# Performance work log

Measured on AMD Instinct MI355X. Metric: run time of the kernel, lower is better.

Reference implementation:

```python
import jax, jax.numpy as jnp
import numpy as np

B, T, E = 4, 1024, 1024
H, MULT = 16, 2
HD = E // H
SCALE = HD ** -0.5


def setup_inputs() -> dict:
    key = jax.random.key(0)
    ks = jax.random.split(key, 9)
    s = 0.02
    return {
        "hidden_states": jax.random.normal(ks[0], (B, T, E), jnp.float32),
        "attention_mask": jnp.zeros((B, 1, T, T), jnp.float32),
        "Wq": jax.random.normal(ks[1], (E, E), jnp.float32) * s,
        "bq": jnp.zeros((E,), jnp.float32),
        "Wk": jax.random.normal(ks[2], (MULT * E, E), jnp.float32) * s,
        "bk": jnp.zeros((MULT * E,), jnp.float32),
        "Wv": jax.random.normal(ks[3], (MULT * E, E), jnp.float32) * s,
        "bv": jnp.zeros((MULT * E,), jnp.float32),
        "Wo": jax.random.normal(ks[4], (E, E), jnp.float32) * s,
        "bo": jnp.zeros((E,), jnp.float32),
    }


def reference(hidden_states, attention_mask, Wq, bq, Wk, bk, Wv, bv, Wo, bo):
    x = hidden_states  # [B, T, E]
    # q projection, scaled
    q = (jnp.einsum("bte,fe->btf", x, Wq) + bq) * SCALE  # [B,T,E]
    q = q.reshape(B, T, H, HD).transpose(0, 2, 1, 3)      # [B,H,T,HD]
    # k/v project to multiplier-expanded dim, then _shape with seq_len=-1:
    # [B,T,MULT*E] -> view(B, T*MULT, H, HD) (torch view semantics) -> [B,H,T*MULT,HD]
    k = jnp.einsum("bte,fe->btf", x, Wk) + bk             # [B,T,MULT*E]
    k = k.reshape(B, T * MULT, H, HD).transpose(0, 2, 1, 3)
    v = jnp.einsum("bte,fe->btf", x, Wv) + bv
    v = v.reshape(B, T * MULT, H, HD).transpose(0, 2, 1, 3)

    S = T * MULT  # src_len; src_len0 = T
    attn = jnp.einsum("bhtd,bhsd->bhts", q, k)            # [B,H,T,S]
    # custom mask broadcast: view src as [MULT, src_len0] and add mask[:, :, :, None, :]
    attn = attn.reshape(B, H, T, MULT, T) + attention_mask[:, :, :, None, :]
    attn = attn.reshape(B, H, T, S)
    attn = jax.nn.softmax(attn, axis=-1)
    out = jnp.einsum("bhts,bhsd->bhtd", attn, v)          # [B,H,T,HD]
    out = out.transpose(0, 2, 1, 3).reshape(B, T, E)
    out = jnp.einsum("bte,fe->btf", out, Wo) + bo
    return out
```

## Files before the change

kernel.cpp:

```cpp
#include <hip/hip_runtime.h>
#include <math.h>

#define BB    4
#define TT    1024
#define EE    1024
#define HH    16
#define HDIM  64
#define SS    2048
#define MROWS 4096
#define SCALEQ 0.125f

typedef short  s8v  __attribute__((ext_vector_type(8)));
typedef float  f4v  __attribute__((ext_vector_type(4)));

__device__ __forceinline__ unsigned short f2bf(float f) {
    union { float f; unsigned u; } c; c.f = f;
    unsigned u = c.u + 0x7FFFu + ((c.u >> 16) & 1u);
    return (unsigned short)(u >> 16);
}
__device__ __forceinline__ float bf2f(unsigned short h) {
    union { unsigned u; float f; } c; c.u = ((unsigned)h) << 16;
    return c.f;
}

__device__ __forceinline__ void async16(const void* g, void* l) {
    __builtin_amdgcn_global_load_lds(
        (const __attribute__((address_space(1))) unsigned int*)g,
        (__attribute__((address_space(3))) unsigned int*)l,
        16, 0, 0);
}

__global__ __launch_bounds__(256) void cvt6_kernel(
    const float* __restrict__ x,  const float* __restrict__ wq,
    const float* __restrict__ wk, const float* __restrict__ wv,
    const float* __restrict__ wo, const float* __restrict__ mk,
    unsigned short* __restrict__ xb,  unsigned short* __restrict__ wqb,
    unsigned short* __restrict__ wkb, unsigned short* __restrict__ wvb,
    unsigned short* __restrict__ wob, unsigned short* __restrict__ mbb)
{
    const int total = 3670016;
    int i = blockIdx.x * 256 + threadIdx.x;
    const int stride = gridDim.x * 256;
    for (; i < total; i += stride) {
        const float* s; unsigned short* d; int off;
        if (i < 1048576)      { s = x;  d = xb;  off = i; }
        else if (i < 1310720) { s = wq; d = wqb; off = i - 1048576; }
        else if (i < 1835008) { s = wk; d = wkb; off = i - 1310720; }
        else if (i < 2359296) { s = wv; d = wvb; off = i - 1835008; }
        else if (i < 2621440) { s = wo; d = wob; off = i - 2359296; }
        else                  { s = mk; d = mbb; off = i - 2621440; }
        float4 v = ((const float4*)s)[off];
        ushort4 o;
        o.x = f2bf(v.x); o.y = f2bf(v.y); o.z = f2bf(v.z); o.w = f2bf(v.w);
        ((ushort4*)d)[off] = o;
    }
}

#define GEMM_KLOOP(Aptr, Wptr, Ksz)                                            \
    for (int k0 = 0; k0 < (Ksz); k0 += 32) {                                   \
        _Pragma("unroll")                                                      \
        for (int it = 0; it < 2; ++it) {                                       \
            int f = (it * 4 + w) * 64 + lane;                                  \
            int r = f >> 2, g = (f & 3) * 8;                                   \
            async16((Aptr) + (size_t)(m0 + r) * (Ksz) + k0 + g,                \
                    As + (it * 4 + w) * 512);                                  \
            async16((Wptr) + (size_t)(n0 + r) * (Ksz) + k0 + g,                \
                    Bs + (it * 4 + w) * 512);                                  \
        }                                                                      \
        __syncthreads();                                                       \
        s8v af[4], bf[4];                                                      \
        _Pragma("unroll")                                                      \
        for (int i = 0; i < 4; ++i)                                            \
            af[i] = *(const s8v*)(As + (wm + i * 16 + col16) * 32 + quad * 8); \
        _Pragma("unroll")                                                      \
        for (int j = 0; j < 4; ++j)                                            \
            bf[j] = *(const s8v*)(Bs + (wn + j * 16 + col16) * 32 + quad * 8); \
        _Pragma("unroll")                                                      \
        for (int i = 0; i < 4; ++i)                                            \
            _Pragma("unroll")                                                  \
            for (int j = 0; j < 4; ++j)                                        \
                acc[i][j] = __builtin_amdgcn_mfma_f32_16x16x32_bf16(           \
                    af[i], bf[j], acc[i][j], 0, 0, 0);                         \
        __syncthreads();                                                       \
    }

__global__ __launch_bounds__(256, 3) void gemm_qk_kernel(
    const unsigned short* __restrict__ X,  const unsigned short* __restrict__ Wq,
    const unsigned short* __restrict__ Wk, const float* __restrict__ bq,
    const float* __restrict__ bk, unsigned short* __restrict__ qp,
    unsigned short* __restrict__ kp)
{
    __shared__ __align__(16) unsigned short As[128 * 32];
    __shared__ __align__(16) unsigned short Bs[128 * 32];

    const int tid = threadIdx.x;
    const int lane = tid & 63, w = tid >> 6;
    const int wm = (w & 1) * 64, wn = (w >> 1) * 64;
    const int col16 = lane & 15, quad = lane >> 4;
    const int m0 = blockIdx.x * 128;
    const bool isQ = blockIdx.y < 8;
    const int n0 = blockIdx.y * 128;
    const unsigned short* Wrow = isQ ? Wq + (size_t)n0 * EE
                                     : Wk + (size_t)(n0 - EE) * EE;

    f4v acc[4][4];
#pragma unroll
    for (int i = 0; i < 4; ++i)
#pragma unroll
        for (int j = 0; j < 4; ++j) acc[i][j] = (f4v)0.0f;

    for (int k0 = 0; k0 < EE; k0 += 32) {
#pragma unroll
        for (int it = 0; it < 2; ++it) {
            int f = (it * 4 + w) * 64 + lane;
            int r = f >> 2, g = (f & 3) * 8;
            async16(X + (size_t)(m0 + r) * EE + k0 + g, As + (it * 4 + w) * 512);
            async16(Wrow + (size_t)r * EE + k0 + g, Bs + (it * 4 + w) * 512);
        }
        __syncthreads();
        s8v af[4], bf[4];
#pragma unroll
        for (int i = 0; i < 4; ++i)
            af[i] = *(const s8v*)(As + (wm + i * 16 + col16) * 32 + quad * 8);
#pragma unroll
        for (int j = 0; j < 4; ++j)
            bf[j] = *(const s8v*)(Bs + (wn + j * 16 + col16) * 32 + quad * 8);
#pragma unroll
        for (int i = 0; i < 4; ++i)
#pragma unroll
            for (int j = 0; j < 4; ++j)
                acc[i][j] = __builtin_amdgcn_mfma_f32_16x16x32_bf16(
                    af[i], bf[j], acc[i][j], 0, 0, 0);
        __syncthreads();
    }

#pragma unroll
    for (int j = 0; j < 4; ++j) {
        const int n = n0 + wn + j * 16 + col16;
        const float bn = isQ ? bq[n] : bk[n - EE];
#pragma unroll
        for (int i = 0; i < 4; ++i) {
            const int mb = m0 + wm + i * 16 + quad * 4;
#pragma unroll
            for (int r = 0; r < 4; ++r) {
                const int m = mb + r;
                float c = acc[i][j][r] + bn;
                if (isQ) {
                    qp[(size_t)m * EE + n] = f2bf(c * SCALEQ);
                } else {
                    const int nk = n - EE;
                    const int mm = nk >> 10, h = (nk >> 6) & 15, d = nk & 63;
                    const int b_ = m >> 10, t = m & 1023;
                    const int s = 2 * t + mm;
                    kp[((size_t)(b_ * HH + h) * SS + s) * HDIM + d] = f2bf(c);
                }
            }
        }
    }
}

template <int LAYOUT, int OUTF32, int Ksz, int Nsz>
__global__ __launch_bounds__(256, 3) void gemm_mfma_kernel(
    const unsigned short* __restrict__ A, const unsigned short* __restrict__ W,
    const float* __restrict__ bias, void* __restrict__ Cout, float alpha)
{
    __shared__ __align__(16) unsigned short As[128 * 32];
    __shared__ __align__(16) unsigned short Bs[128 * 32];

    const int tid = threadIdx.x;
    const int lane = tid & 63, w = tid >> 6;
    const int wm = (w & 1) * 64, wn = (w >> 1) * 64;
    const int col16 = lane & 15, quad = lane >> 4;
    const int m0 = blockIdx.x * 128;
    const int n0 = blockIdx.y * 128;

    f4v acc[4][4];
#pragma unroll
    for (int i = 0; i < 4; ++i)
#pragma unroll
        for (int j = 0; j < 4; ++j) acc[i][j] = (f4v)0.0f;

    GEMM_KLOOP(A, W, Ksz)

#pragma unroll
    for (int j = 0; j < 4; ++j) {
        const int n = n0 + wn + j * 16 + col16;
        const float bn = (LAYOUT == 2) ? 0.0f : bias[n];
#pragma unroll
        for (int i = 0; i < 4; ++i) {
            const int mb = m0 + wm + i * 16 + quad * 4;
#pragma unroll
            for (int r = 0; r < 4; ++r) {
                const int m = mb + r;
                float c = (acc[i][j][r] + ((LAYOUT == 2) ? bias[m] : bn)) * alpha;
                if (LAYOUT == 0) {
                    if (OUTF32) ((float*)Cout)[(size_t)m * Nsz + n] = c;
                    else ((unsigned short*)Cout)[(size_t)m * Nsz + n] = f2bf(c);
                } else {
                    const int mm = m >> 10, h = (m >> 6) & 15, d = m & 63;
                    const int b_ = n >> 10, t = n & 1023;
                    const int s = 2 * t + mm;
                    ((unsigned short*)Cout)[((size_t)(b_ * HH + h) * HDIM + d) * SS + s] = f2bf(c);
                }
            }
        }
    }
}

__global__ __launch_bounds__(256, 3) void attn_mfma2_kernel(
    const unsigned short* __restrict__ Q, const unsigned short* __restrict__ Kh,
    const unsigned short* __restrict__ Vt, const unsigned short* __restrict__ Mb,
    unsigned short* __restrict__ O)
{
    constexpr int PT = 68;
    __shared__ __align__(16) unsigned short Qs[64 * PT];
    __shared__ __align__(16) unsigned short K0[64 * PT];
    __shared__ __align__(16) unsigned short K1[64 * PT];
    __shared__ __align__(16) unsigned short V0[64 * PT];
    __shared__ __align__(16) unsigned short V1[64 * PT];
    __shared__ __align__(16) unsigned short Ms[64 * PT];

    const int tid = threadIdx.x;
    const int lane = tid & 63, w = tid >> 6;
    const int col16 = lane & 15, quad = lane >> 4;

    const int gid = blockIdx.x;
    const int v = gid & 7, j = gid >> 3;
    const int bh = v * 8 + (j >> 4);
    const int t0 = (j & 15) * 64;
    const int b_ = bh >> 4, h = bh & 15;

#pragma unroll
    for (int it = 0; it < 2; ++it) {
        int idx = tid + it * 256;
        int r = idx >> 3, c = (idx & 7) * 8;
        *(uint4*)(Qs + r * PT + c) =
            *(const uint4*)(Q + (size_t)(b_ * TT + t0 + r) * EE + h * HDIM + c);
    }

    f4v oacc[4];
#pragma unroll
    for (int jd = 0; jd < 4; ++jd) oacc[jd] = (f4v)0.0f;
    float mrun = -INFINITY, lrun = 0.0f;

    const unsigned short* Kb  = Kh + (size_t)bh * SS * HDIM;
    const unsigned short* Vb  = Vt + (size_t)bh * HDIM * SS;
    const unsigned short* Mbb = Mb + (size_t)b_ * TT * TT;
    const int myrow = (w * 16 + col16) * PT;

    for (int it16 = 0; it16 < 16; ++it16) {
        const int t2b = it16 * 64;
        __syncthreads();
#pragma unroll
        for (int st = 0; st < 2; ++st) {
            int idx = tid + st * 256;
            int r = idx >> 3, c = (idx & 7) * 8;
            *(uint4*)(K0 + r * PT + c) = *(const uint4*)(Kb + (size_t)(t2b + r) * HDIM + c);
            *(uint4*)(K1 + r * PT + c) = *(const uint4*)(Kb + (size_t)(1024 + t2b + r) * HDIM + c);
            *(uint4*)(V0 + r * PT + c) = *(const uint4*)(Vb + (size_t)r * SS + t2b + c);
            *(uint4*)(V1 + r * PT + c) = *(const uint4*)(Vb + (size_t)r * SS + 1024 + t2b + c);
            *(uint4*)(Ms + r * PT + c) = *(const uint4*)(Mbb + (size_t)(t0 + r) * TT + t2b + c);
        }
        __syncthreads();

        f4v s0acc[4], s1acc[4];
#pragma unroll
        for (int js = 0; js < 4; ++js) { s0acc[js] = (f4v)0.0f; s1acc[js] = (f4v)0.0f; }
#pragma unroll
        for (int ks = 0; ks < 2; ++ks) {
            s8v bq_ = *(const s8v*)(Qs + myrow + ks * 32 + quad * 8);
#pragma unroll
            for (int js = 0; js < 4; ++js) {
                s8v ak0 = *(const s8v*)(K0 + (js * 16 + col16) * PT + ks * 32 + quad * 8);
                s8v ak1 = *(const s8v*)(K1 + (js * 16 + col16) * PT + ks * 32 + quad * 8);
                s0acc[js] = __builtin_amdgcn_mfma_f32_16x16x32_bf16(ak0, bq_, s0acc[js], 0, 0, 0);
                s1acc[js] = __builtin_amdgcn_mfma_f32_16x16x32_bf16(ak1, bq_, s1acc[js], 0, 0, 0);
            }
        }

#pragma unroll
        for (int js = 0; js < 4; ++js) {
            uint2 mm = *(const uint2*)(Ms + myrow + js * 16 + quad * 4);
            float m0f = bf2f((unsigned short)(mm.x & 0xffff));
            float m1f = bf2f((unsigned short)(mm.x >> 16));
            float m2f = bf2f((unsigned short)(mm.y & 0xffff));
            float m3f = bf2f((unsigned short)(mm.y >> 16));
            s0acc[js][0] += m0f; s1acc[js][0] += m0f;
            s0acc[js][1] += m1f; s1acc[js][1] += m1f;
            s0acc[js][2] += m2f; s1acc[js][2] += m2f;
            s0acc[js][3] += m3f; s1acc[js][3] += m3f;
        }

        float tmax = -INFINITY;
#pragma unroll
        for (int js = 0; js < 4; ++js)
#pragma unroll
            for (int r = 0; r < 4; ++r)
                tmax = fmaxf(tmax, fmaxf(s0acc[js][r], s1acc[js][r]));
        tmax = fmaxf(tmax, __shfl_xor(tmax, 16));
        tmax = fmaxf(tmax, __shfl_xor(tmax, 32));
        const float mnew = fmaxf(mrun, tmax);
        const float scl = __expf(mrun - mnew);
        float rs = 0.0f;
#pragma unroll
        for (int js = 0; js < 4; ++js)
#pragma unroll
            for (int r = 0; r < 4; ++r) {
                float p0 = __expf(s0acc[js][r] - mnew);
                float p1 = __expf(s1acc[js][r] - mnew);
                s0acc[js][r] = p0; s1acc[js][r] = p1;
                rs += p0 + p1;
            }
        rs += __shfl_xor(rs, 16);
        rs += __shfl_xor(rs, 32);
        lrun = lrun * scl + rs;
        mrun = mnew;

        float sclr[4];
#pragma unroll
        for (int r = 0; r < 4; ++r) sclr[r] = __shfl(scl, quad * 4 + r);
#pragma unroll
        for (int jd = 0; jd < 4; ++jd)
#pragma unroll
            for (int r = 0; r < 4; ++r) oacc[jd][r] *= sclr[r];

        __syncthreads();

#pragma unroll
        for (int js = 0; js < 4; ++js) {
            unsigned p01 = (unsigned)f2bf(s0acc[js][0]) | ((unsigned)f2bf(s0acc[js][1]) << 16);
            unsigned p23 = (unsigned)f2bf(s0acc[js][2]) | ((unsigned)f2bf(s0acc[js][3]) << 16);
            *(uint2*)(K0 + myrow + js * 16 + quad * 4) = make_uint2(p01, p23);
            p01 = (unsigned)f2bf(s1acc[js][0]) | ((unsigned)f2bf(s1acc[js][1]) << 16);
            p23 = (unsigned)f2bf(s1acc[js][2]) | ((unsigned)f2bf(s1acc[js][3]) << 16);
            *(uint2*)(K1 + myrow + js * 16 + quad * 4) = make_uint2(p01, p23);
        }
        __syncthreads();

#pragma unroll
        for (int ks = 0; ks < 2; ++ks) {
            s8v p0 = *(const s8v*)(K0 + myrow + ks * 32 + quad * 8);
            s8v p1 = *(const s8v*)(K1 + myrow + ks * 32 + quad * 8);
#pragma unroll
            for (int jd = 0; jd < 4; ++jd) {
                s8v v0_ = *(const s8v*)(V0 + (jd * 16 + col16) * PT + ks * 32 + quad * 8);
                s8v v1_ = *(const s8v*)(V1 + (jd * 16 + col16) * PT + ks * 32 + quad * 8);
                oacc[jd] = __builtin_amdgcn_mfma_f32_16x16x32_bf16(p0, v0_, oacc[jd], 0, 0, 0);
                oacc[jd] = __builtin_amdgcn_mfma_f32_16x16x32_bf16(p1, v1_, oacc[jd], 0, 0, 0);
            }
        }
    }

    const float inv = 1.0f / lrun;
    float invr[4];
#pragma unroll
    for (int r = 0; r < 4; ++r) invr[r] = __shfl(inv, quad * 4 + r);
#pragma unroll
    for (int r = 0; r < 4; ++r) {
        const int t = t0 + w * 16 + quad * 4 + r;
#pragma unroll
        for (int jd = 0; jd < 4; ++jd)
            O[(size_t)(b_ * TT + t) * EE + h * HDIM + jd * 16 + col16] =
                f2bf(oacc[jd][r] * invr[r]);
    }
}

extern "C" void kernel_launch(void* const* d_in, const int* in_sizes, int n_in,
                              void* d_out, int out_size, void* d_ws, size_t ws_size,
                              hipStream_t stream)
{
    (void)in_sizes; (void)n_in; (void)out_size; (void)ws_size;

    const float* x    = (const float*)d_in[0];
    const float* mask = (const float*)d_in[1];
    const float* Wq   = (const float*)d_in[2];
    const float* bq   = (const float*)d_in[3];
    const float* Wk   = (const float*)d_in[4];
    const float* bk   = (const float*)d_in[5];
    const float* Wv   = (const float*)d_in[6];
    const float* bv   = (const float*)d_in[7];
    const float* Wo   = (const float*)d_in[8];
    const float* bo   = (const float*)d_in[9];
    float* out = (float*)d_out;

    unsigned short* xb  = (unsigned short*)d_ws;
    unsigned short* wqb = xb  + (size_t)MROWS * EE;
    unsigned short* wkb = wqb + (size_t)EE * EE;
    unsigned short* wvb = wkb + (size_t)2 * EE * EE;
    unsigned short* wob = wvb + (size_t)2 * EE * EE;
    unsigned short* mb  = wob + (size_t)EE * EE;
    unsigned short* qp  = mb  + (size_t)BB * TT * TT;
    unsigned short* kp  = qp  + (size_t)MROWS * EE;
    unsigned short* vt  = kp  + (size_t)BB * HH * SS * HDIM;
    unsigned short* ao  = vt  + (size_t)BB * HH * SS * HDIM;

    dim3 blk(256);

    cvt6_kernel<<<4096, blk, 0, stream>>>(x, Wq, Wk, Wv, Wo, mask,
                                          xb, wqb, wkb, wvb, wob, mb);
    gemm_qk_kernel<<<dim3(32, 24), blk, 0, stream>>>(xb, wqb, wkb, bq, bk, qp, kp);
    gemm_mfma_kernel<2, 0, EE, MROWS><<<dim3(16, 32), blk, 0, stream>>>(
        wvb, xb, bv, vt, 1.0f);
    attn_mfma2_kernel<<<dim3(1024), blk, 0, stream>>>(qp, kp, vt, mb, ao);
    gemm_mfma_kernel<0, 1, EE, EE><<<dim3(32, 8), blk, 0, stream>>>(
        ao, wob, bo, out, 1.0f);
}
```

Measured before the change: 287.7 us.

## Fuse Q/K/V projection GEMMs and switch attention to 32x32 MFMA tiles

Merges the separate QK and V projection GEMM launches into one 1280-block kernel that picks its operands and output layout from the block index, removing one launch and its tail. The attention kernel is rewritten to use 32x32x16 bf16 MFMA with 128-query tiles per block, so each K/V tile loaded into shared memory is reused by twice as many queries and the row-max and row-sum reductions need fewer cross-lane shuffles. Shared memory use per block grows and the occupancy hint drops from 3 to 2 blocks per CU, which may reduce latency hiding.

```diff
diff --git a/kernel.cpp b/kernel.cpp
--- a/kernel.cpp
+++ b/kernel.cpp
@@ -12,6 +12,7 @@
 
 typedef short  s8v  __attribute__((ext_vector_type(8)));
 typedef float  f4v  __attribute__((ext_vector_type(4)));
+typedef float  f16v __attribute__((ext_vector_type(16)));
 
 __device__ __forceinline__ unsigned short f2bf(float f) {
     union { float f; unsigned u; } c; c.f = f;
@@ -62,9 +63,9 @@
         for (int it = 0; it < 2; ++it) {                                       \
             int f = (it * 4 + w) * 64 + lane;                                  \
             int r = f >> 2, g = (f & 3) * 8;                                   \
-            async16((Aptr) + (size_t)(m0 + r) * (Ksz) + k0 + g,                \
+            async16((Aptr) + (size_t)r * (Ksz) + k0 + g,                       \
                     As + (it * 4 + w) * 512);                                  \
-            async16((Wptr) + (size_t)(n0 + r) * (Ksz) + k0 + g,                \
+            async16((Wptr) + (size_t)r * (Ksz) + k0 + g,                       \
                     Bs + (it * 4 + w) * 512);                                  \
         }                                                                      \
         __syncthreads();                                                       \
@@ -84,11 +85,14 @@
         __syncthreads();                                                       \
     }
 
-__global__ __launch_bounds__(256, 3) void gemm_qk_kernel(
-    const unsigned short* __restrict__ X,  const unsigned short* __restrict__ Wq,
-    const unsigned short* __restrict__ Wk, const float* __restrict__ bq,
-    const float* __restrict__ bk, unsigned short* __restrict__ qp,
-    unsigned short* __restrict__ kp)
+__global__ __launch_bounds__(256, 3) void gemm_qkv_kernel(
+    const unsigned short* __restrict__ X,
+    const unsigned short* __restrict__ Wq, const unsigned short* __restrict__ Wk,
+    const unsigned short* __restrict__ Wv,
+    const float* __restrict__ bq, const float* __restrict__ bk,
+    const float* __restrict__ bv,
+    unsigned short* __restrict__ qp, unsigned short* __restrict__ kp,
+    unsigned short* __restrict__ vt)
 {
     __shared__ __align__(16) unsigned short As[128 * 32];
     __shared__ __align__(16) unsigned short Bs[128 * 32];
@@ -97,11 +101,20 @@
     const int lane = tid & 63, w = tid >> 6;
     const int wm = (w & 1) * 64, wn = (w >> 1) * 64;
     const int col16 = lane & 15, quad = lane >> 4;
-    const int m0 = blockIdx.x * 128;
-    const bool isQ = blockIdx.y < 8;
-    const int n0 = blockIdx.y * 128;
-    const unsigned short* Wrow = isQ ? Wq + (size_t)n0 * EE
-                                     : Wk + (size_t)(n0 - EE) * EE;
+
+    const int gid = blockIdx.x;
+    int mode, mi, ni;
+    const unsigned short *Ab, *Bb;
+    if (gid < 256) {
+        mode = 0; mi = gid >> 3; ni = gid & 7;
+        Ab = X + (size_t)mi * 128 * EE;  Bb = Wq + (size_t)ni * 128 * EE;
+    } else if (gid < 768) {
+        int g = gid - 256; mode = 1; mi = g >> 4; ni = g & 15;
+        Ab = X + (size_t)mi * 128 * EE;  Bb = Wk + (size_t)ni * 128 * EE;
+    } else {
+        int g = gid - 768; mode = 2; mi = g & 15; ni = g >> 4;
+        Ab = Wv + (size_t)mi * 128 * EE; Bb = X + (size_t)ni * 128 * EE;
+    }
 
     f4v acc[4][4];
 #pragma unroll
@@ -109,57 +122,39 @@
 #pragma unroll
         for (int j = 0; j < 4; ++j) acc[i][j] = (f4v)0.0f;
 
-    for (int k0 = 0; k0 < EE; k0 += 32) {
-#pragma unroll
-        for (int it = 0; it < 2; ++it) {
-            int f = (it * 4 + w) * 64 + lane;
-            int r = f >> 2, g = (f & 3) * 8;
-            async16(X + (size_t)(m0 + r) * EE + k0 + g, As + (it * 4 + w) * 512);
-            async16(Wrow + (size_t)r * EE + k0 + g, Bs + (it * 4 + w) * 512);
-        }
-        __syncthreads();
-        s8v af[4], bf[4];
-#pragma unroll
-        for (int i = 0; i < 4; ++i)
-            af[i] = *(const s8v*)(As + (wm + i * 16 + col16) * 32 + quad * 8);
-#pragma unroll
-        for (int j = 0; j < 4; ++j)
-            bf[j] = *(const s8v*)(Bs + (wn + j * 16 + col16) * 32 + quad * 8);
-#pragma unroll
-        for (int i = 0; i < 4; ++i)
-#pragma unroll
-            for (int j = 0; j < 4; ++j)
-                acc[i][j] = __builtin_amdgcn_mfma_f32_16x16x32_bf16(
-                    af[i], bf[j], acc[i][j], 0, 0, 0);
-        __syncthreads();
-    }
+    GEMM_KLOOP(Ab, Bb, EE)
 
 #pragma unroll
     for (int j = 0; j < 4; ++j) {
-        const int n = n0 + wn + j * 16 + col16;
-        const float bn = isQ ? bq[n] : bk[n - EE];
+        const int nl = wn + j * 16 + col16;
 #pragma unroll
         for (int i = 0; i < 4; ++i) {
-            const int mb = m0 + wm + i * 16 + quad * 4;
 #pragma unroll
             for (int r = 0; r < 4; ++r) {
-                const int m = mb + r;
-                float c = acc[i][j][r] + bn;
-                if (isQ) {
-                    qp[(size_t)m * EE + n] = f2bf(c * SCALEQ);
-                } else {
-                    const int nk = n - EE;
+                const int ml = wm + i * 16 + quad * 4 + r;
+                float c = acc[i][j][r];
+                if (mode == 0) {
+                    const int m = mi * 128 + ml, n = ni * 128 + nl;
+                    qp[(size_t)m * EE + n] = f2bf((c + bq[n]) * SCALEQ);
+                } else if (mode == 1) {
+                    const int m = mi * 128 + ml, nk = ni * 128 + nl;
                     const int mm = nk >> 10, h = (nk >> 6) & 15, d = nk & 63;
                     const int b_ = m >> 10, t = m & 1023;
                     const int s = 2 * t + mm;
-                    kp[((size_t)(b_ * HH + h) * SS + s) * HDIM + d] = f2bf(c);
+                    kp[((size_t)(b_ * HH + h) * SS + s) * HDIM + d] = f2bf(c + bk[nk]);
+                } else {
+                    const int f = mi * 128 + ml, tok = ni * 128 + nl;
+                    const int mm = f >> 10, h = (f >> 6) & 15, d = f & 63;
+                    const int b_ = tok >> 10, t = tok & 1023;
+                    const int s = 2 * t + mm;
+                    vt[((size_t)(b_ * HH + h) * HDIM + d) * SS + s] = f2bf(c + bv[f]);
                 }
             }
         }
     }
 }
 
-template <int LAYOUT, int OUTF32, int Ksz, int Nsz>
+template <int OUTF32, int Ksz, int Nsz>
 __global__ __launch_bounds__(256, 3) void gemm_mfma_kernel(
     const unsigned short* __restrict__ A, const unsigned short* __restrict__ W,
     const float* __restrict__ bias, void* __restrict__ Cout, float alpha)
@@ -171,8 +166,8 @@
     const int lane = tid & 63, w = tid >> 6;
     const int wm = (w & 1) * 64, wn = (w >> 1) * 64;
     const int col16 = lane & 15, quad = lane >> 4;
-    const int m0 = blockIdx.x * 128;
-    const int n0 = blockIdx.y * 128;
+    const unsigned short* Ab = A + (size_t)blockIdx.x * 128 * Ksz;
+    const unsigned short* Bb = W + (size_t)blockIdx.y * 128 * Ksz;
 
     f4v acc[4][4];
 #pragma unroll
@@ -180,124 +175,130 @@
 #pragma unroll
         for (int j = 0; j < 4; ++j) acc[i][j] = (f4v)0.0f;
 
-    GEMM_KLOOP(A, W, Ksz)
+    GEMM_KLOOP(Ab, Bb, Ksz)
 
 #pragma unroll
     for (int j = 0; j < 4; ++j) {
-        const int n = n0 + wn + j * 16 + col16;
-        const float bn = (LAYOUT == 2) ? 0.0f : bias[n];
+        const int n = blockIdx.y * 128 + wn + j * 16 + col16;
+        const float bn = bias[n];
 #pragma unroll
         for (int i = 0; i < 4; ++i) {
-            const int mb = m0 + wm + i * 16 + quad * 4;
 #pragma unroll
             for (int r = 0; r < 4; ++r) {
-                const int m = mb + r;
-                float c = (acc[i][j][r] + ((LAYOUT == 2) ? bias[m] : bn)) * alpha;
-                if (LAYOUT == 0) {
-                    if (OUTF32) ((float*)Cout)[(size_t)m * Nsz + n] = c;
-                    else ((unsigned short*)Cout)[(size_t)m * Nsz + n] = f2bf(c);
-                } else {
-                    const int mm = m >> 10, h = (m >> 6) & 15, d = m & 63;
-                    const int b_ = n >> 10, t = n & 1023;
-                    const int s = 2 * t + mm;
-                    ((unsigned short*)Cout)[((size_t)(b_ * HH + h) * HDIM + d) * SS + s] = f2bf(c);
-                }
-            }
-        }
-    }
-}
-
-__global__ __launch_bounds__(256, 3) void attn_mfma2_kernel(
+                const int m = blockIdx.x * 128 + wm + i * 16 + quad * 4 + r;
+                float c = (acc[i][j][r] + bn) * alpha;
+                if (OUTF32) ((float*)Cout)[(size_t)m * Nsz + n] = c;
+                else ((unsigned short*)Cout)[(size_t)m * Nsz + n] = f2bf(c);
+            }
+        }
+    }
+}
+
+__global__ __launch_bounds__(256, 2) void attn_mfma32_kernel(
     const unsigned short* __restrict__ Q, const unsigned short* __restrict__ Kh,
     const unsigned short* __restrict__ Vt, const unsigned short* __restrict__ Mb,
     unsigned short* __restrict__ O)
 {
     constexpr int PT = 68;
-    __shared__ __align__(16) unsigned short Qs[64 * PT];
-    __shared__ __align__(16) unsigned short K0[64 * PT];
-    __shared__ __align__(16) unsigned short K1[64 * PT];
-    __shared__ __align__(16) unsigned short V0[64 * PT];
-    __shared__ __align__(16) unsigned short V1[64 * PT];
-    __shared__ __align__(16) unsigned short Ms[64 * PT];
+    constexpr int PP = 132;
+    __shared__ __align__(16) unsigned short Qs[128 * PT];
+    __shared__ __align__(16) unsigned short KM[256 * PT];
+    __shared__ __align__(16) unsigned short V0s[64 * PT];
+    __shared__ __align__(16) unsigned short V1s[64 * PT];
 
     const int tid = threadIdx.x;
     const int lane = tid & 63, w = tid >> 6;
-    const int col16 = lane & 15, quad = lane >> 4;
+    const int l31 = lane & 31;
+    const int h8 = (lane >> 5) * 8;
+    const int h4 = (lane >> 5) * 4;
 
     const int gid = blockIdx.x;
     const int v = gid & 7, j = gid >> 3;
-    const int bh = v * 8 + (j >> 4);
-    const int t0 = (j & 15) * 64;
+    const int bh = v * 8 + (j & 7);
+    const int t0 = (j >> 3) * 128;
     const int b_ = bh >> 4, h = bh & 15;
 
-#pragma unroll
-    for (int it = 0; it < 2; ++it) {
-        int idx = tid + it * 256;
+    unsigned short* K0 = KM;
+    unsigned short* K1 = KM + 64 * PT;
+    unsigned short* Ms = KM + 128 * PT;
+    unsigned short* P  = KM;
+
+#pragma unroll
+    for (int st = 0; st < 4; ++st) {
+        int idx = tid + st * 256;
         int r = idx >> 3, c = (idx & 7) * 8;
         *(uint4*)(Qs + r * PT + c) =
             *(const uint4*)(Q + (size_t)(b_ * TT + t0 + r) * EE + h * HDIM + c);
     }
 
-    f4v oacc[4];
-#pragma unroll
-    for (int jd = 0; jd < 4; ++jd) oacc[jd] = (f4v)0.0f;
+    f16v oacc[2];
+    oacc[0] = (f16v)0.0f; oacc[1] = (f16v)0.0f;
     float mrun = -INFINITY, lrun = 0.0f;
 
     const unsigned short* Kb  = Kh + (size_t)bh * SS * HDIM;
     const unsigned short* Vb  = Vt + (size_t)bh * HDIM * SS;
     const unsigned short* Mbb = Mb + (size_t)b_ * TT * TT;
-    const int myrow = (w * 16 + col16) * PT;
-
-    for (int it16 = 0; it16 < 16; ++it16) {
-        const int t2b = it16 * 64;
+
+    const int trow = w * 32 + l31;
+    const int qrow = trow * PT;
+    const int prow = trow * PP;
+
+    for (int it = 0; it < 16; ++it) {
+        const int t2b = it * 64;
         __syncthreads();
 #pragma unroll
         for (int st = 0; st < 2; ++st) {
             int idx = tid + st * 256;
             int r = idx >> 3, c = (idx & 7) * 8;
-            *(uint4*)(K0 + r * PT + c) = *(const uint4*)(Kb + (size_t)(t2b + r) * HDIM + c);
-            *(uint4*)(K1 + r * PT + c) = *(const uint4*)(Kb + (size_t)(1024 + t2b + r) * HDIM + c);
-            *(uint4*)(V0 + r * PT + c) = *(const uint4*)(Vb + (size_t)r * SS + t2b + c);
-            *(uint4*)(V1 + r * PT + c) = *(const uint4*)(Vb + (size_t)r * SS + 1024 + t2b + c);
+            *(uint4*)(K0 + r * PT + c)  = *(const uint4*)(Kb + (size_t)(t2b + r) * HDIM + c);
+            *(uint4*)(K1 + r * PT + c)  = *(const uint4*)(Kb + (size_t)(1024 + t2b + r) * HDIM + c);
+            *(uint4*)(V0s + r * PT + c) = *(const uint4*)(Vb + (size_t)r * SS + t2b + c);
+            *(uint4*)(V1s + r * PT + c) = *(const uint4*)(Vb + (size_t)r * SS + 1024 + t2b + c);
+        }
+#pragma unroll
+        for (int st = 0; st < 4; ++st) {
+            int idx = tid + st * 256;
+            int r = idx >> 3, c = (idx & 7) * 8;
             *(uint4*)(Ms + r * PT + c) = *(const uint4*)(Mbb + (size_t)(t0 + r) * TT + t2b + c);
         }
         __syncthreads();
 
-        f4v s0acc[4], s1acc[4];
-#pragma unroll
-        for (int js = 0; js < 4; ++js) { s0acc[js] = (f4v)0.0f; s1acc[js] = (f4v)0.0f; }
-#pragma unroll
-        for (int ks = 0; ks < 2; ++ks) {
-            s8v bq_ = *(const s8v*)(Qs + myrow + ks * 32 + quad * 8);
+        f16v sacc[4];
+#pragma unroll
+        for (int js = 0; js < 4; ++js) sacc[js] = (f16v)0.0f;
+#pragma unroll
+        for (int kk = 0; kk < 4; ++kk) {
+            s8v qf = *(const s8v*)(Qs + qrow + kk * 16 + h8);
 #pragma unroll
             for (int js = 0; js < 4; ++js) {
-                s8v ak0 = *(const s8v*)(K0 + (js * 16 + col16) * PT + ks * 32 + quad * 8);
-                s8v ak1 = *(const s8v*)(K1 + (js * 16 + col16) * PT + ks * 32 + quad * 8);
-                s0acc[js] = __builtin_amdgcn_mfma_f32_16x16x32_bf16(ak0, bq_, s0acc[js], 0, 0, 0);
-                s1acc[js] = __builtin_amdgcn_mfma_f32_16x16x32_bf16(ak1, bq_, s1acc[js], 0, 0, 0);
-            }
-        }
-
-#pragma unroll
-        for (int js = 0; js < 4; ++js) {
-            uint2 mm = *(const uint2*)(Ms + myrow + js * 16 + quad * 4);
-            float m0f = bf2f((unsigned short)(mm.x & 0xffff));
-            float m1f = bf2f((unsigned short)(mm.x >> 16));
-            float m2f = bf2f((unsigned short)(mm.y & 0xffff));
-            float m3f = bf2f((unsigned short)(mm.y >> 16));
-            s0acc[js][0] += m0f; s1acc[js][0] += m0f;
-            s0acc[js][1] += m1f; s1acc[js][1] += m1f;
-            s0acc[js][2] += m2f; s1acc[js][2] += m2f;
-            s0acc[js][3] += m3f; s1acc[js][3] += m3f;
-        }
+                const unsigned short* kt = (js < 2) ? K0 : K1;
+                s8v kf = *(const s8v*)(kt + ((js & 1) * 32 + l31) * PT + kk * 16 + h8);
+                sacc[js] = __builtin_amdgcn_mfma_f32_32x32x16_bf16(kf, qf, sacc[js], 0, 0, 0);
+            }
+        }
+
+        uint2 mu[2][4];
+#pragma unroll
+        for (int jh = 0; jh < 2; ++jh)
+#pragma unroll
+            for (int q = 0; q < 4; ++q)
+                mu[jh][q] = *(const uint2*)(Ms + qrow + jh * 32 + 8 * q + h4);
+#pragma unroll
+        for (int js = 0; js < 4; ++js)
+#pragma unroll
+            for (int q = 0; q < 4; ++q) {
+                uint2 m2 = mu[js & 1][q];
+                sacc[js][4 * q + 0] += bf2f((unsigned short)(m2.x & 0xffff));
+                sacc[js][4 * q + 1] += bf2f((unsigned short)(m2.x >> 16));
+                sacc[js][4 * q + 2] += bf2f((unsigned short)(m2.y & 0xffff));
+                sacc[js][4 * q + 3] += bf2f((unsigned short)(m2.y >> 16));
+            }
 
         float tmax = -INFINITY;
 #pragma unroll
         for (int js = 0; js < 4; ++js)
 #pragma unroll
-            for (int r = 0; r < 4; ++r)
-                tmax = fmaxf(tmax, fmaxf(s0acc[js][r], s1acc[js][r]));
-        tmax = fmaxf(tmax, __shfl_xor(tmax, 16));
+            for (int e = 0; e < 16; ++e) tmax = fmaxf(tmax, sacc[js][e]);
         tmax = fmaxf(tmax, __shfl_xor(tmax, 32));
         const float mnew = fmaxf(mrun, tmax);
         const float scl = __expf(mrun - mnew);
@@ -305,64 +306,56 @@
 #pragma unroll
         for (int js = 0; js < 4; ++js)
 #pragma unroll
-            for (int r = 0; r < 4; ++r) {
-                float p0 = __expf(s0acc[js][r] - mnew);
-                float p1 = __expf(s1acc[js][r] - mnew);
-                s0acc[js][r] = p0; s1acc[js][r] = p1;
-                rs += p0 + p1;
-            }
-        rs += __shfl_xor(rs, 16);
+            for (int e = 0; e < 16; ++e) {
+                float p = __expf(sacc[js][e] - mnew);
+                sacc[js][e] = p;
+                rs += p;
+            }
         rs += __shfl_xor(rs, 32);
         lrun = lrun * scl + rs;
         mrun = mnew;
-
-        float sclr[4];
-#pragma unroll
-        for (int r = 0; r < 4; ++r) sclr[r] = __shfl(scl, quad * 4 + r);
-#pragma unroll
-        for (int jd = 0; jd < 4; ++jd)
-#pragma unroll
-            for (int r = 0; r < 4; ++r) oacc[jd][r] *= sclr[r];
+        oacc[0] *= scl;
+        oacc[1] *= scl;
 
         __syncthreads();
 
 #pragma unroll
-        for (int js = 0; js < 4; ++js) {
-            unsigned p01 = (unsigned)f2bf(s0acc[js][0]) | ((unsigned)f2bf(s0acc[js][1]) << 16);
-            unsigned p23 = (unsigned)f2bf(s0acc[js][2]) | ((unsigned)f2bf(s0acc[js][3]) << 16);
-            *(uint2*)(K0 + myrow + js * 16 + quad * 4) = make_uint2(p01, p23);
-            p01 = (unsigned)f2bf(s1acc[js][0]) | ((unsigned)f2bf(s1acc[js][1]) << 16);
-            p23 = (unsigned)f2bf(s1acc[js][2]) | ((unsigned)f2bf(s1acc[js][3]) << 16);
-            *(uint2*)(K1 + myrow + js * 16 + quad * 4) = make_uint2(p01, p23);
-        }
+        for (int js = 0; js < 4; ++js)
+#pragma unroll
+            for (int q = 0; q < 4; ++q) {
+                unsigned p01 = (unsigned)f2bf(sacc[js][4 * q + 0]) |
+                               ((unsigned)f2bf(sacc[js][4 * q + 1]) << 16);
+                unsigned p23 = (unsigned)f2bf(sacc[js][4 * q + 2]) |
+                               ((unsigned)f2bf(sacc[js][4 * q + 3]) << 16);
+                *(uint2*)(P + prow + js * 32 + 8 * q + h4) = make_uint2(p01, p23);
+            }
         __syncthreads();
 
 #pragma unroll
-        for (int ks = 0; ks < 2; ++ks) {
-            s8v p0 = *(const s8v*)(K0 + myrow + ks * 32 + quad * 8);
-            s8v p1 = *(const s8v*)(K1 + myrow + ks * 32 + quad * 8);
-#pragma unroll
-            for (int jd = 0; jd < 4; ++jd) {
-                s8v v0_ = *(const s8v*)(V0 + (jd * 16 + col16) * PT + ks * 32 + quad * 8);
-                s8v v1_ = *(const s8v*)(V1 + (jd * 16 + col16) * PT + ks * 32 + quad * 8);
-                oacc[jd] = __builtin_amdgcn_mfma_f32_16x16x32_bf16(p0, v0_, oacc[jd], 0, 0, 0);
-                oacc[jd] = __builtin_amdgcn_mfma_f32_16x16x32_bf16(p1, v1_, oacc[jd], 0, 0, 0);
-            }
+        for (int ks = 0; ks < 8; ++ks) {
+            const unsigned short* vtile = (ks < 4) ? V0s : V1s;
+            const int ko = (ks & 3) * 16 + h8;
+            s8v pf  = *(const s8v*)(P + prow + ks * 16 + h8);
+            s8v vf0 = *(const s8v*)(vtile + l31 * PT + ko);
+            s8v vf1 = *(const s8v*)(vtile + (32 + l31) * PT + ko);
+            oacc[0] = __builtin_amdgcn_mfma_f32_32x32x16_bf16(vf0, pf, oacc[0], 0, 0, 0);
+            oacc[1] = __builtin_amdgcn_mfma_f32_32x32x16_bf16(vf1, pf, oacc[1], 0, 0, 0);
         }
     }
 
     const float inv = 1.0f / lrun;
-    float invr[4];
-#pragma unroll
-    for (int r = 0; r < 4; ++r) invr[r] = __shfl(inv, quad * 4 + r);
-#pragma unroll
-    for (int r = 0; r < 4; ++r) {
-        const int t = t0 + w * 16 + quad * 4 + r;
-#pragma unroll
-        for (int jd = 0; jd < 4; ++jd)
-            O[(size_t)(b_ * TT + t) * EE + h * HDIM + jd * 16 + col16] =
-                f2bf(oacc[jd][r] * invr[r]);
-    }
+    const int tg = t0 + trow;
+#pragma unroll
+    for (int jd = 0; jd < 2; ++jd)
+#pragma unroll
+        for (int q = 0; q < 4; ++q) {
+            unsigned p01 = (unsigned)f2bf(oacc[jd][4 * q + 0] * inv) |
+                           ((unsigned)f2bf(oacc[jd][4 * q + 1] * inv) << 16);
+            unsigned p23 = (unsigned)f2bf(oacc[jd][4 * q + 2] * inv) |
+                           ((unsigned)f2bf(oacc[jd][4 * q + 3] * inv) << 16);
+            *(uint2*)(O + (size_t)(b_ * TT + tg) * EE + h * HDIM + jd * 32 + 8 * q + h4) =
+                make_uint2(p01, p23);
+        }
 }
 
 extern "C" void kernel_launch(void* const* d_in, const int* in_sizes, int n_in,
@@ -398,10 +391,9 @@
 
     cvt6_kernel<<<4096, blk, 0, stream>>>(x, Wq, Wk, Wv, Wo, mask,
                                           xb, wqb, wkb, wvb, wob, mb);
-    gemm_qk_kernel<<<dim3(32, 24), blk, 0, stream>>>(xb, wqb, wkb, bq, bk, qp, kp);
-    gemm_mfma_kernel<2, 0, EE, MROWS><<<dim3(16, 32), blk, 0, stream>>>(
-        wvb, xb, bv, vt, 1.0f);
-    attn_mfma2_kernel<<<dim3(1024), blk, 0, stream>>>(qp, kp, vt, mb, ao);
-    gemm_mfma_kernel<0, 1, EE, EE><<<dim3(32, 8), blk, 0, stream>>>(
+    gemm_qkv_kernel<<<dim3(1280), blk, 0, stream>>>(
+        xb, wqb, wkb, wvb, bq, bk, bv, qp, kp, vt);
+    attn_mfma32_kernel<<<dim3(512), blk, 0, stream>>>(qp, kp, vt, mb, ao);
+    gemm_mfma_kernel<1, EE, EE><<<dim3(32, 8), blk, 0, stream>>>(
         ao, wob, bo, out, 1.0f);
 }
```

Result: slower. 396.2 us (+37.7%).

## Fuse Q/K/V projections into one launch and stream Q, V from registers/global

Applied to the files above, without the earlier changes.

Merges the separate Q/K GEMM and V GEMM into a single 1280-block kernel that dispatches by block index to the Q, K or transposed-V epilogue, removing one launch and letting all tiles share the GPU at once. The attention kernel now keeps Q fragments in registers and reads V fragments directly from global memory instead of staging Q, V0 and V1 in LDS. This cuts LDS use and raises the occupancy hint to 4. The trade-off is uncoalesced, uncached-in-LDS global loads of V inside the inner loop, which could raise memory latency.

```diff
diff --git a/kernel.cpp b/kernel.cpp
--- a/kernel.cpp
+++ b/kernel.cpp
@@ -62,9 +62,9 @@
         for (int it = 0; it < 2; ++it) {                                       \
             int f = (it * 4 + w) * 64 + lane;                                  \
             int r = f >> 2, g = (f & 3) * 8;                                   \
-            async16((Aptr) + (size_t)(m0 + r) * (Ksz) + k0 + g,                \
+            async16((Aptr) + (size_t)r * (Ksz) + k0 + g,                       \
                     As + (it * 4 + w) * 512);                                  \
-            async16((Wptr) + (size_t)(n0 + r) * (Ksz) + k0 + g,                \
+            async16((Wptr) + (size_t)r * (Ksz) + k0 + g,                       \
                     Bs + (it * 4 + w) * 512);                                  \
         }                                                                      \
         __syncthreads();                                                       \
@@ -84,11 +84,14 @@
         __syncthreads();                                                       \
     }
 
-__global__ __launch_bounds__(256, 3) void gemm_qk_kernel(
-    const unsigned short* __restrict__ X,  const unsigned short* __restrict__ Wq,
-    const unsigned short* __restrict__ Wk, const float* __restrict__ bq,
-    const float* __restrict__ bk, unsigned short* __restrict__ qp,
-    unsigned short* __restrict__ kp)
+__global__ __launch_bounds__(256, 4) void gemm_qkv_kernel(
+    const unsigned short* __restrict__ X,
+    const unsigned short* __restrict__ Wq, const unsigned short* __restrict__ Wk,
+    const unsigned short* __restrict__ Wv,
+    const float* __restrict__ bq, const float* __restrict__ bk,
+    const float* __restrict__ bv,
+    unsigned short* __restrict__ qp, unsigned short* __restrict__ kp,
+    unsigned short* __restrict__ vt)
 {
     __shared__ __align__(16) unsigned short As[128 * 32];
     __shared__ __align__(16) unsigned short Bs[128 * 32];
@@ -97,11 +100,20 @@
     const int lane = tid & 63, w = tid >> 6;
     const int wm = (w & 1) * 64, wn = (w >> 1) * 64;
     const int col16 = lane & 15, quad = lane >> 4;
-    const int m0 = blockIdx.x * 128;
-    const bool isQ = blockIdx.y < 8;
-    const int n0 = blockIdx.y * 128;
-    const unsigned short* Wrow = isQ ? Wq + (size_t)n0 * EE
-                                     : Wk + (size_t)(n0 - EE) * EE;
+
+    const int gid = blockIdx.x;
+    int mode, mi, ni;
+    const unsigned short *Ab, *Bb;
+    if (gid < 256) {
+        mode = 0; mi = gid >> 3; ni = gid & 7;
+        Ab = X + (size_t)mi * 128 * EE;  Bb = Wq + (size_t)ni * 128 * EE;
+    } else if (gid < 768) {
+        int g = gid - 256; mode = 1; mi = g >> 4; ni = g & 15;
+        Ab = X + (size_t)mi * 128 * EE;  Bb = Wk + (size_t)ni * 128 * EE;
+    } else {
+        int g = gid - 768; mode = 2; mi = g & 15; ni = g >> 4;
+        Ab = Wv + (size_t)mi * 128 * EE; Bb = X + (size_t)ni * 128 * EE;
+    }
 
     f4v acc[4][4];
 #pragma unroll
@@ -109,57 +121,39 @@
 #pragma unroll
         for (int j = 0; j < 4; ++j) acc[i][j] = (f4v)0.0f;
 
-    for (int k0 = 0; k0 < EE; k0 += 32) {
-#pragma unroll
-        for (int it = 0; it < 2; ++it) {
-            int f = (it * 4 + w) * 64 + lane;
-            int r = f >> 2, g = (f & 3) * 8;
-            async16(X + (size_t)(m0 + r) * EE + k0 + g, As + (it * 4 + w) * 512);
-            async16(Wrow + (size_t)r * EE + k0 + g, Bs + (it * 4 + w) * 512);
-        }
-        __syncthreads();
-        s8v af[4], bf[4];
-#pragma unroll
-        for (int i = 0; i < 4; ++i)
-            af[i] = *(const s8v*)(As + (wm + i * 16 + col16) * 32 + quad * 8);
-#pragma unroll
-        for (int j = 0; j < 4; ++j)
-            bf[j] = *(const s8v*)(Bs + (wn + j * 16 + col16) * 32 + quad * 8);
-#pragma unroll
-        for (int i = 0; i < 4; ++i)
-#pragma unroll
-            for (int j = 0; j < 4; ++j)
-                acc[i][j] = __builtin_amdgcn_mfma_f32_16x16x32_bf16(
-                    af[i], bf[j], acc[i][j], 0, 0, 0);
-        __syncthreads();
-    }
+    GEMM_KLOOP(Ab, Bb, EE)
 
 #pragma unroll
     for (int j = 0; j < 4; ++j) {
-        const int n = n0 + wn + j * 16 + col16;
-        const float bn = isQ ? bq[n] : bk[n - EE];
+        const int nl = wn + j * 16 + col16;
 #pragma unroll
         for (int i = 0; i < 4; ++i) {
-            const int mb = m0 + wm + i * 16 + quad * 4;
 #pragma unroll
             for (int r = 0; r < 4; ++r) {
-                const int m = mb + r;
-                float c = acc[i][j][r] + bn;
-                if (isQ) {
-                    qp[(size_t)m * EE + n] = f2bf(c * SCALEQ);
-                } else {
-                    const int nk = n - EE;
+                const int ml = wm + i * 16 + quad * 4 + r;
+                float c = acc[i][j][r];
+                if (mode == 0) {
+                    const int m = mi * 128 + ml, n = ni * 128 + nl;
+                    qp[(size_t)m * EE + n] = f2bf((c + bq[n]) * SCALEQ);
+                } else if (mode == 1) {
+                    const int m = mi * 128 + ml, nk = ni * 128 + nl;
                     const int mm = nk >> 10, h = (nk >> 6) & 15, d = nk & 63;
                     const int b_ = m >> 10, t = m & 1023;
                     const int s = 2 * t + mm;
-                    kp[((size_t)(b_ * HH + h) * SS + s) * HDIM + d] = f2bf(c);
+                    kp[((size_t)(b_ * HH + h) * SS + s) * HDIM + d] = f2bf(c + bk[nk]);
+                } else {
+                    const int f = mi * 128 + ml, tok = ni * 128 + nl;
+                    const int mm = f >> 10, h = (f >> 6) & 15, d = f & 63;
+                    const int b_ = tok >> 10, t = tok & 1023;
+                    const int s = 2 * t + mm;
+                    vt[((size_t)(b_ * HH + h) * HDIM + d) * SS + s] = f2bf(c + bv[f]);
                 }
             }
         }
     }
 }
 
-template <int LAYOUT, int OUTF32, int Ksz, int Nsz>
+template <int OUTF32, int Ksz, int Nsz>
 __global__ __launch_bounds__(256, 3) void gemm_mfma_kernel(
     const unsigned short* __restrict__ A, const unsigned short* __restrict__ W,
     const float* __restrict__ bias, void* __restrict__ Cout, float alpha)
@@ -171,8 +165,8 @@
     const int lane = tid & 63, w = tid >> 6;
     const int wm = (w & 1) * 64, wn = (w >> 1) * 64;
     const int col16 = lane & 15, quad = lane >> 4;
-    const int m0 = blockIdx.x * 128;
-    const int n0 = blockIdx.y * 128;
+    const unsigned short* Ab = A + (size_t)blockIdx.x * 128 * Ksz;
+    const unsigned short* Bb = W + (size_t)blockIdx.y * 128 * Ksz;
 
     f4v acc[4][4];
 #pragma unroll
@@ -180,44 +174,33 @@
 #pragma unroll
         for (int j = 0; j < 4; ++j) acc[i][j] = (f4v)0.0f;
 
-    GEMM_KLOOP(A, W, Ksz)
+    GEMM_KLOOP(Ab, Bb, Ksz)
 
 #pragma unroll
     for (int j = 0; j < 4; ++j) {
-        const int n = n0 + wn + j * 16 + col16;
-        const float bn = (LAYOUT == 2) ? 0.0f : bias[n];
+        const int n = blockIdx.y * 128 + wn + j * 16 + col16;
+        const float bn = bias[n];
 #pragma unroll
         for (int i = 0; i < 4; ++i) {
-            const int mb = m0 + wm + i * 16 + quad * 4;
 #pragma unroll
             for (int r = 0; r < 4; ++r) {
-                const int m = mb + r;
-                float c = (acc[i][j][r] + ((LAYOUT == 2) ? bias[m] : bn)) * alpha;
-                if (LAYOUT == 0) {
-                    if (OUTF32) ((float*)Cout)[(size_t)m * Nsz + n] = c;
-                    else ((unsigned short*)Cout)[(size_t)m * Nsz + n] = f2bf(c);
-                } else {
-                    const int mm = m >> 10, h = (m >> 6) & 15, d = m & 63;
-                    const int b_ = n >> 10, t = n & 1023;
-                    const int s = 2 * t + mm;
-                    ((unsigned short*)Cout)[((size_t)(b_ * HH + h) * HDIM + d) * SS + s] = f2bf(c);
-                }
-            }
-        }
-    }
-}
-
-__global__ __launch_bounds__(256, 3) void attn_mfma2_kernel(
+                const int m = blockIdx.x * 128 + wm + i * 16 + quad * 4 + r;
+                float c = (acc[i][j][r] + bn) * alpha;
+                if (OUTF32) ((float*)Cout)[(size_t)m * Nsz + n] = c;
+                else ((unsigned short*)Cout)[(size_t)m * Nsz + n] = f2bf(c);
+            }
+        }
+    }
+}
+
+__global__ __launch_bounds__(256, 4) void attn_mfma4_kernel(
     const unsigned short* __restrict__ Q, const unsigned short* __restrict__ Kh,
     const unsigned short* __restrict__ Vt, const unsigned short* __restrict__ Mb,
     unsigned short* __restrict__ O)
 {
     constexpr int PT = 68;
-    __shared__ __align__(16) unsigned short Qs[64 * PT];
     __shared__ __align__(16) unsigned short K0[64 * PT];
     __shared__ __align__(16) unsigned short K1[64 * PT];
-    __shared__ __align__(16) unsigned short V0[64 * PT];
-    __shared__ __align__(16) unsigned short V1[64 * PT];
     __shared__ __align__(16) unsigned short Ms[64 * PT];
 
     const int tid = threadIdx.x;
@@ -230,23 +213,20 @@
     const int t0 = (j & 15) * 64;
     const int b_ = bh >> 4, h = bh & 15;
 
-#pragma unroll
-    for (int it = 0; it < 2; ++it) {
-        int idx = tid + it * 256;
-        int r = idx >> 3, c = (idx & 7) * 8;
-        *(uint4*)(Qs + r * PT + c) =
-            *(const uint4*)(Q + (size_t)(b_ * TT + t0 + r) * EE + h * HDIM + c);
-    }
-
-    f4v oacc[4];
-#pragma unroll
-    for (int jd = 0; jd < 4; ++jd) oacc[jd] = (f4v)0.0f;
-    float mrun = -INFINITY, lrun = 0.0f;
-
     const unsigned short* Kb  = Kh + (size_t)bh * SS * HDIM;
     const unsigned short* Vb  = Vt + (size_t)bh * HDIM * SS;
     const unsigned short* Mbb = Mb + (size_t)b_ * TT * TT;
     const int myrow = (w * 16 + col16) * PT;
+
+    const unsigned short* Qrow = Q + (size_t)(b_ * TT + t0 + w * 16 + col16) * EE + h * HDIM;
+    s8v qf[2];
+    qf[0] = *(const s8v*)(Qrow + quad * 8);
+    qf[1] = *(const s8v*)(Qrow + 32 + quad * 8);
+
+    f4v oacc[4];
+#pragma unroll
+    for (int jd = 0; jd < 4; ++jd) oacc[jd] = (f4v)0.0f;
+    float mrun = -INFINITY, lrun = 0.0f;
 
     for (int it16 = 0; it16 < 16; ++it16) {
         const int t2b = it16 * 64;
@@ -257,8 +237,6 @@
             int r = idx >> 3, c = (idx & 7) * 8;
             *(uint4*)(K0 + r * PT + c) = *(const uint4*)(Kb + (size_t)(t2b + r) * HDIM + c);
             *(uint4*)(K1 + r * PT + c) = *(const uint4*)(Kb + (size_t)(1024 + t2b + r) * HDIM + c);
-            *(uint4*)(V0 + r * PT + c) = *(const uint4*)(Vb + (size_t)r * SS + t2b + c);
-            *(uint4*)(V1 + r * PT + c) = *(const uint4*)(Vb + (size_t)r * SS + 1024 + t2b + c);
             *(uint4*)(Ms + r * PT + c) = *(const uint4*)(Mbb + (size_t)(t0 + r) * TT + t2b + c);
         }
         __syncthreads();
@@ -268,7 +246,7 @@
         for (int js = 0; js < 4; ++js) { s0acc[js] = (f4v)0.0f; s1acc[js] = (f4v)0.0f; }
 #pragma unroll
         for (int ks = 0; ks < 2; ++ks) {
-            s8v bq_ = *(const s8v*)(Qs + myrow + ks * 32 + quad * 8);
+            s8v bq_ = qf[ks];
 #pragma unroll
             for (int js = 0; js < 4; ++js) {
                 s8v ak0 = *(const s8v*)(K0 + (js * 16 + col16) * PT + ks * 32 + quad * 8);
@@ -343,8 +321,9 @@
             s8v p1 = *(const s8v*)(K1 + myrow + ks * 32 + quad * 8);
 #pragma unroll
             for (int jd = 0; jd < 4; ++jd) {
-                s8v v0_ = *(const s8v*)(V0 + (jd * 16 + col16) * PT + ks * 32 + quad * 8);
-                s8v v1_ = *(const s8v*)(V1 + (jd * 16 + col16) * PT + ks * 32 + quad * 8);
+                const unsigned short* vrow = Vb + (size_t)(jd * 16 + col16) * SS;
+                s8v v0_ = *(const s8v*)(vrow + t2b + ks * 32 + quad * 8);
+                s8v v1_ = *(const s8v*)(vrow + 1024 + t2b + ks * 32 + quad * 8);
                 oacc[jd] = __builtin_amdgcn_mfma_f32_16x16x32_bf16(p0, v0_, oacc[jd], 0, 0, 0);
                 oacc[jd] = __builtin_amdgcn_mfma_f32_16x16x32_bf16(p1, v1_, oacc[jd], 0, 0, 0);
             }
@@ -398,10 +377,9 @@
 
     cvt6_kernel<<<4096, blk, 0, stream>>>(x, Wq, Wk, Wv, Wo, mask,
                                           xb, wqb, wkb, wvb, wob, mb);
-    gemm_qk_kernel<<<dim3(32, 24), blk, 0, stream>>>(xb, wqb, wkb, bq, bk, qp, kp);
-    gemm_mfma_kernel<2, 0, EE, MROWS><<<dim3(16, 32), blk, 0, stream>>>(
-        wvb, xb, bv, vt, 1.0f);
-    attn_mfma2_kernel<<<dim3(1024), blk, 0, stream>>>(qp, kp, vt, mb, ao);
-    gemm_mfma_kernel<0, 1, EE, EE><<<dim3(32, 8), blk, 0, stream>>>(
+    gemm_qkv_kernel<<<dim3(1280), blk, 0, stream>>>(
+        xb, wqb, wkb, wvb, bq, bk, bv, qp, kp, vt);
+    attn_mfma4_kernel<<<dim3(1024), blk, 0, stream>>>(qp, kp, vt, mb, ao);
+    gemm_mfma_kernel<1, EE, EE><<<dim3(32, 8), blk, 0, stream>>>(
         ao, wob, bo, out, 1.0f);
 }
```

Result: slower. 343.9 us (+19.5%).
